# Kernel optimization log

Measured on AMD Instinct MI355X. Metric: run time of the kernel, lower is better.

The kernel has to match this reference:

```python
import jax, jax.numpy as jnp
import numpy as np

B, C, T, N = 8, 128, 12, 4096
E_HALF = 131072
EPS = 1e-5


def _linear_params(key, fan_in, fan_out):
    kw, kb = jax.random.split(key)
    bound = 1.0 / np.sqrt(fan_in)
    W = jax.random.uniform(kw, (fan_in, fan_out), jnp.float32, -bound, bound)
    b = jax.random.uniform(kb, (fan_out,), jnp.float32, -bound, bound)
    return W, b


def setup_inputs() -> dict:
    key = jax.random.key(0)
    ks = jax.random.split(key, 10)
    h_in = jax.random.normal(ks[0], (B, C, T, N), jnp.float32)
    # symmetric edge list: random pairs + reverses + self loops
    u = jax.random.randint(ks[1], (E_HALF,), 0, N, jnp.int32)
    v = jax.random.randint(ks[2], (E_HALF,), 0, N, jnp.int32)
    loops = jnp.arange(N, dtype=jnp.int32)
    row = jnp.concatenate([u, v, loops])
    col = jnp.concatenate([v, u, loops])
    edge_index = jnp.stack([row, col])  # [2, E]
    Wq, bq = _linear_params(ks[3], C, C)
    Wk, bk = _linear_params(ks[4], C, C)
    Wv, bv = _linear_params(ks[5], C, C)
    W1, b1 = _linear_params(ks[6], 2 * C, 4 * C)
    W2, b2 = _linear_params(ks[7], 4 * C, C)
    W3, b3 = _linear_params(ks[8], C, 1)
    return dict(h_in=h_in, edge_index=edge_index, Wq=Wq, bq=bq, Wk=Wk, bk=bk,
                Wv=Wv, bv=bv, W1=W1, b1=b1, W2=W2, b2=b2, W3=W3, b3=b3)


def _masked_instance_norm(x, mask_f):
    # stats over the non-self-loop edges only (matching torch, where the MLP
    # only sees edge_index[:, non_self_loop_mask])
    cnt = mask_f.sum()
    mean = (x * mask_f).sum(0) / cnt
    var = (((x - mean) ** 2) * mask_f).sum(0) / cnt
    return (x - mean) / jnp.sqrt(var + EPS)


def _forward(h_in, edge_index, Wq, bq, Wk, bk, Wv, bv, W1, b1, W2, b2, W3, b3):
    # ---- TemporalAttention ----
    x = jnp.transpose(h_in, (0, 3, 2, 1))  # [B, N, T, C]
    q = x @ Wq + bq
    k = x @ Wk + bk
    v = x @ Wv + bv
    scores = jnp.einsum('bntc,bnsc->bnts', q, k) / (C ** 0.5)
    attn = jax.nn.softmax(scores, axis=-1)
    weighted = jnp.einsum('bnts,bnsc->bntc', attn, v)
    emb = weighted.sum(axis=2)          # [B, N, C]
    emb_mean = emb.mean(axis=0)         # [N, C]

    # ---- ExtractorMLP on non-self-loop edges ----
    row, col = edge_index[0], edge_index[1]
    self_loop = row == col
    mask_f = (~self_loop).astype(emb_mean.dtype)[:, None]  # [E, 1]
    f12 = jnp.concatenate([emb_mean[row], emb_mean[col]], axis=-1)  # [E, 2C]
    h = jax.nn.relu(_masked_instance_norm(f12 @ W1 + b1, mask_f))
    h = jax.nn.relu(_masked_instance_norm(h @ W2 + b2, mask_f))
    logits = h @ W3 + b3                 # [E, 1]

    # concrete_sample, eval mode (deterministic)
    att = jax.nn.sigmoid(logits)
    all_att = jnp.where(self_loop[:, None], 1.0, att)  # [E, 1]

    # ---- transpose + reorder_like: match each edge with its reverse ----
    M = jnp.max(edge_index) + 1
    fwd_key = row * M + col
    rev_key = col * M + row
    order = jnp.argsort(fwd_key)
    pos = jnp.searchsorted(fwd_key[order], rev_key)
    perm = order[pos]                    # index of reverse edge
    edge_att = (all_att + all_att[perm]) * 0.5
    return edge_att


def reference(h_in, edge_index, Wq, bq, Wk, bk, Wv, bv, W1, b1, W2, b2, W3, b3):
    return _forward(h_in, edge_index, Wq, bq, Wk, bk, Wv, bv, W1, b1, W2, b2, W3, b3)
```

## Files before the change

### kernel.cpp

```cpp
#include <hip/hip_runtime.h>
#include <hip/hip_bf16.h>

#define CC     128
#define TT     12
#define NNODE  4096
#define NE     266240
#define EHALF  131072
#define F1     512
#define EPS    1e-5f
#define RSQRTC 0.08838834764831845f
#define EBG    48
#define NBLKG2 5547
#define NF2B   87
#define ST     40

#define O_XWM   0ull
#define O_ICNT  524288ull
#define O_CNT   524416ull
#define O_T     528512ull
#define O_S     528640ull
#define O_T2    545024ull
#define O_GTB   561408ull
#define O_W0B   569600ull
#define O_WC1   569664ull
#define O_WC2   635200ull
#define O_B1C   700736ull
#define O_M1    701248ull
#define O_IS1   701760ull
#define O_M2    702272ull
#define O_IS2   702400ull
#define O_W2T   702528ull
#define O_PB    735296ull
#define O_QB    1783872ull
#define O_ALLA  2832448ull
#define O_PART  3098688ull
#define O_PART2 4518720ull
#define O_Z2    4540992ull

typedef __attribute__((ext_vector_type(8))) short bf16x8;
typedef __attribute__((ext_vector_type(4))) float f32x4;

__device__ inline float bfbits2f(unsigned int v) { return __uint_as_float(v << 16); }
__device__ inline unsigned short f2bf(float x) {
  union { __hip_bfloat16 h; unsigned short u; } cv;
  cv.h = __float2bfloat16(x);
  return cv.u;
}
__device__ inline float f4get(const float4& v, int k) {
  return k == 0 ? v.x : k == 1 ? v.y : k == 2 ? v.z : v.w;
}

__global__ void k_pre(const float* __restrict__ Wq, const float* __restrict__ bq,
                      const float* __restrict__ Wk,
                      unsigned short* __restrict__ Gtb, unsigned short* __restrict__ w0b) {
  int i = blockIdx.x, j = threadIdx.x;
  float acc = 0.f;
  for (int co = 0; co < CC; ++co) acc = fmaf(Wq[i*CC+co], Wk[j*CC+co], acc);
  Gtb[j*CC + i] = f2bf(acc);
  if (j == 0) {
    float a = 0.f;
    for (int co = 0; co < CC; ++co) a = fmaf(Wk[i*CC+co], bq[co], a);
    w0b[i] = f2bf(a);
  }
}

__global__ __launch_bounds__(256) void k_prew(const float* __restrict__ Wv,
    const float* __restrict__ bv, const float* __restrict__ W1, const float* __restrict__ b1,
    float* __restrict__ Wc1, float* __restrict__ Wc2, float* __restrict__ b1c) {
  __shared__ float wvr[CC];
  const int c = blockIdx.x, tid = threadIdx.x;
  if (tid < CC) wvr[tid] = Wv[(size_t)c*CC + tid];
  __syncthreads();
  for (int h = 0; h < 2; ++h) {
    int f = h*256 + tid;
    float a1 = 0.f, a2 = 0.f;
    for (int j = 0; j < CC; ++j) {
      float wv = wvr[j];
      a1 = fmaf(wv, W1[(size_t)j*F1 + f], a1);
      a2 = fmaf(wv, W1[(size_t)(CC + j)*F1 + f], a2);
    }
    Wc1[(size_t)c*F1 + f] = a1;
    Wc2[(size_t)c*F1 + f] = a2;
  }
  if (c == 0) {
    for (int h = 0; h < 2; ++h) {
      int f = h*256 + tid;
      float s = b1[f];
      for (int j = 0; j < CC; ++j)
        s = fmaf(12.f*bv[j], W1[(size_t)j*F1 + f] + W1[(size_t)(CC + j)*F1 + f], s);
      b1c[f] = s;
    }
  }
}

__global__ void k_w2t(const float* __restrict__ W2, unsigned short* __restrict__ W2T) {
  int n = blockIdx.x;
  for (int k = threadIdx.x; k < F1; k += 256)
    W2T[(size_t)n*F1 + k] = f2bf(W2[(size_t)k*CC + n]);
}

__global__ __launch_bounds__(256) void k_hist(const int* __restrict__ row,
    const int* __restrict__ col, int* __restrict__ cnt, int* __restrict__ icnt) {
  __shared__ int h[NNODE];
  const int tid = threadIdx.x;
  for (int i = tid; i < NNODE; i += 256) h[i] = 0;
  __syncthreads();
  int lc = 0;
  const int base = blockIdx.x << 12;
  for (int i = tid; i < 4096; i += 256) {
    int e = base + i;
    int r = row[e], c = col[e];
    if (r != c) { atomicAdd(&h[r], 1); ++lc; }
  }
  #pragma unroll
  for (int d = 1; d < 64; d <<= 1) lc += __shfl_xor(lc, d);
  __syncthreads();
  for (int i = tid; i < NNODE; i += 256) { int v = h[i]; if (v) atomicAdd(&cnt[i], v); }
  if ((tid & 63) == 0) atomicAdd(icnt, lc);
}

__global__ __launch_bounds__(256, 8) void k_attn(
    const float* __restrict__ h_in,
    const unsigned short* __restrict__ Gtb,
    const unsigned short* __restrict__ w0b,
    float* __restrict__ xwm) {
  __shared__ unsigned short xs[48*128];
  __shared__ unsigned short ys[48*128];
  const int tid = threadIdx.x;
  const int bid = ((blockIdx.x & 7) << 10) | (blockIdx.x >> 3);
  const int b  = bid >> 10;
  const int n0 = (bid & 1023) << 2;

  const int w = tid >> 6, lane = tid & 63;
  const int l15 = lane & 15, l4 = lane >> 4;

  {
    const int c2 = tid & 63;
    const float* g0 = h_in + (((size_t)b*CC + 2*c2)*TT + w)*NNODE + n0;
    float4 av[3], bv[3];
    #pragma unroll
    for (int it = 0; it < 3; ++it) {
      av[it] = *(const float4*)(g0 + (size_t)(4*it)*NNODE);
      bv[it] = *(const float4*)(g0 + (size_t)(TT + 4*it)*NNODE);
    }
    #pragma unroll
    for (int it = 0; it < 3; ++it) {
      int t = w + it*4;
      #pragma unroll
      for (int i = 0; i < 4; ++i) {
        float xa = f4get(av[it], i);
        float xb = f4get(bv[it], i);
        int r = i*TT + t;
        unsigned byte = ((unsigned)r << 8) + (((unsigned)(c2*4)) ^ (((unsigned)(r & 7)) << 4));
        *(unsigned*)((char*)xs + byte) = (unsigned)f2bf(xa) | ((unsigned)f2bf(xb) << 16);
      }
    }
  }
  __syncthreads();

  {
    f32x4 acc[2][3];
    #pragma unroll
    for (int mt = 0; mt < 2; ++mt)
      #pragma unroll
      for (int nt = 0; nt < 3; ++nt) acc[mt][nt] = (f32x4){0.f,0.f,0.f,0.f};

    #pragma unroll
    for (int kt = 0; kt < 4; ++kt) {
      bf16x8 gf[2];
      #pragma unroll
      for (int mt = 0; mt < 2; ++mt)
        gf[mt] = *(const bf16x8*)(Gtb + (size_t)((w<<5) + (mt<<4) + l15)*CC + (kt<<5) + (l4<<3));
      bf16x8 bfr[3];
      #pragma unroll
      for (int nt = 0; nt < 3; ++nt) {
        int rr = nt*16 + l15;
        unsigned byte = ((unsigned)rr << 8) +
                        (((unsigned)((kt<<6) + (l4<<4))) ^ (((unsigned)(rr & 7)) << 4));
        bfr[nt] = *(const bf16x8*)((const char*)xs + byte);
      }
      #pragma unroll
      for (int mt = 0; mt < 2; ++mt)
        #pragma unroll
        for (int nt = 0; nt < 3; ++nt)
          acc[mt][nt] = __builtin_amdgcn_mfma_f32_16x16x32_bf16(gf[mt], bfr[nt], acc[mt][nt], 0, 0, 0);
    }
    #pragma unroll
    for (int mt = 0; mt < 2; ++mt)
      #pragma unroll
      for (int nt = 0; nt < 3; ++nt) {
        int rr = nt*16 + l15;
        ushort4 v;
        v.x = f2bf(acc[mt][nt][0]); v.y = f2bf(acc[mt][nt][1]);
        v.z = f2bf(acc[mt][nt][2]); v.w = f2bf(acc[mt][nt][3]);
        unsigned cb = (unsigned)((w<<6) + (mt<<5) + (l4<<3));
        unsigned byte = ((unsigned)rr << 8) + (cb ^ (((unsigned)(rr & 7)) << 4));
        *(ushort4*)((char*)ys + byte) = v;
      }
  }
  __syncthreads();

  {
    const int rb = w*TT;
    const bool sval = (l15 < TT);
    const int rr = rb + (sval ? l15 : 0);
    f32x4 sa = (f32x4){0.f,0.f,0.f,0.f};
    #pragma unroll
    for (int kt = 0; kt < 4; ++kt) {
      unsigned byte = ((unsigned)rr << 8) +
                      (((unsigned)((kt<<6) + (l4<<4))) ^ (((unsigned)(rr & 7)) << 4));
      bf16x8 afr = *(const bf16x8*)((const char*)ys + byte);
      bf16x8 bfr = *(const bf16x8*)((const char*)xs + byte);
      sa = __builtin_amdgcn_mfma_f32_16x16x32_bf16(afr, bfr, sa, 0, 0, 0);
    }
    float dloc = 0.f;
    #pragma unroll
    for (int u = 0; u < 4; ++u) {
      unsigned cb = (unsigned)((l4 << 6) + (u << 4));
      unsigned byte = ((unsigned)rr << 8) + (cb ^ (((unsigned)(rr & 7)) << 4));
      bf16x8 xv = *(const bf16x8*)((const char*)xs + byte);
      bf16x8 wv = *(const bf16x8*)(w0b + (l4 << 5) + (u << 3));
      #pragma unroll
      for (int k = 0; k < 8; ++k)
        dloc = fmaf(bfbits2f((unsigned short)xv[k]), bfbits2f((unsigned short)wv[k]), dloc);
    }
    dloc += __shfl_xor(dloc, 16);
    dloc += __shfl_xor(dloc, 32);
    const float dv = dloc;
    float p[4];
    #pragma unroll
    for (int r = 0; r < 4; ++r) {
      float t1 = sval ? (sa[r] + dv) * RSQRTC : -1e30f;
      float m = t1;
      m = fmaxf(m, __shfl_xor(m, 1));
      m = fmaxf(m, __shfl_xor(m, 2));
      m = fmaxf(m, __shfl_xor(m, 4));
      m = fmaxf(m, __shfl_xor(m, 8));
      float e = exp2f((t1 - m) * 1.4426950408889634f);
      float s = e;
      s += __shfl_xor(s, 1);
      s += __shfl_xor(s, 2);
      s += __shfl_xor(s, 4);
      s += __shfl_xor(s, 8);
      p[r] = e / s;
    }
    float wpart = (l4 < 3) ? (p[0] + p[1] + p[2] + p[3]) : 0.f;
    wpart += __shfl_xor(wpart, 16);
    wpart += __shfl_xor(wpart, 32);
    float xw0 = 0.f, xw1 = 0.f;
    #pragma unroll
    for (int s = 0; s < TT; ++s) {
      float wv = __shfl(wpart, s);
      int r2 = rb + s;
      unsigned byte = ((unsigned)r2 << 8) +
                      (((unsigned)(lane << 2)) ^ (((unsigned)(r2 & 7)) << 4));
      unsigned xp = *(const unsigned*)((const char*)xs + byte);
      xw0 = fmaf(wv, bfbits2f(xp & 0xffffu), xw0);
      xw1 = fmaf(wv, bfbits2f(xp >> 16), xw1);
    }
    unsafeAtomicAdd(&xwm[(size_t)(n0 + w)*CC + (lane << 1)],     xw0 * 0.125f);
    unsafeAtomicAdd(&xwm[(size_t)(n0 + w)*CC + (lane << 1) + 1], xw1 * 0.125f);
  }
}

__global__ __launch_bounds__(256) void k_S(const float* __restrict__ xwm,
    const int* __restrict__ row, const int* __restrict__ col, float* __restrict__ S) {
  __shared__ unsigned short XT[128*ST];
  __shared__ unsigned short YT[128*ST];
  const int tid = threadIdx.x;
  const int w = tid >> 6, lane = tid & 63, l15 = lane & 15, l4 = lane >> 4;
  const int j = tid & 31, fi = tid >> 5;
  const int f0 = fi << 4;
  f32x4 acc[2][8];
  #pragma unroll
  for (int mt = 0; mt < 2; ++mt)
    #pragma unroll
    for (int nt = 0; nt < 8; ++nt) acc[mt][nt] = (f32x4){0.f,0.f,0.f,0.f};

  const int ebase = blockIdx.x << 9;
  for (int bt = 0; bt < 16; ++bt) {
    const int e = ebase + (bt << 5) + j;
    const int r = row[e], c = col[e];
    const bool msk = (r != c);
    const float* xr = xwm + (size_t)r*CC + f0;
    const float* xc = xwm + (size_t)c*CC + f0;
    float4 xv[4], yv[4];
    #pragma unroll
    for (int u = 0; u < 4; ++u) { xv[u] = *(const float4*)(xr + 4*u); yv[u] = *(const float4*)(xc + 4*u); }
    __syncthreads();
    #pragma unroll
    for (int u = 0; u < 16; ++u) {
      float xvv = f4get(xv[u >> 2], u & 3);
      float yvv = f4get(yv[u >> 2], u & 3);
      XT[(f0+u)*ST + j] = f2bf(xvv);
      YT[(f0+u)*ST + j] = msk ? f2bf(yvv) : (unsigned short)0;
    }
    __syncthreads();
    bf16x8 af[2];
    #pragma unroll
    for (int mt = 0; mt < 2; ++mt)
      af[mt] = *(const bf16x8*)&XT[((((w<<1)+mt)<<4) + l15)*ST + (l4<<3)];
    #pragma unroll
    for (int nt = 0; nt < 8; ++nt) {
      bf16x8 bf_ = *(const bf16x8*)&YT[(((nt<<4) + l15))*ST + (l4<<3)];
      acc[0][nt] = __builtin_amdgcn_mfma_f32_16x16x32_bf16(af[0], bf_, acc[0][nt], 0, 0, 0);
      acc[1][nt] = __builtin_amdgcn_mfma_f32_16x16x32_bf16(af[1], bf_, acc[1][nt], 0, 0, 0);
    }
  }
  #pragma unroll
  for (int mt = 0; mt < 2; ++mt)
    #pragma unroll
    for (int nt = 0; nt < 8; ++nt)
      #pragma unroll
      for (int reg = 0; reg < 4; ++reg) {
        int a = (((w<<1)+mt)<<4) + (l4<<2) + reg;
        int b = (nt<<4) + l15;
        unsafeAtomicAdd(&S[a*128 + b], acc[mt][nt][reg]);
      }
}

__global__ __launch_bounds__(256) void k_T2(const float* __restrict__ xwm,
    const int* __restrict__ cnt, float* __restrict__ T2, float* __restrict__ t) {
  __shared__ unsigned short XT[128*ST];
  __shared__ unsigned short YT[128*ST];
  __shared__ float tl[128];
  const int tid = threadIdx.x;
  const int w = tid >> 6, lane = tid & 63, l15 = lane & 15, l4 = lane >> 4;
  const int j = tid & 31, fi = tid >> 5;
  const int f0 = fi << 4;
  if (tid < 128) tl[tid] = 0.f;
  f32x4 acc[2][8];
  #pragma unroll
  for (int mt = 0; mt < 2; ++mt)
    #pragma unroll
    for (int nt = 0; nt < 8; ++nt) acc[mt][nt] = (f32x4){0.f,0.f,0.f,0.f};
  float tloc[16];
  #pragma unroll
  for (int u = 0; u < 16; ++u) tloc[u] = 0.f;

  const int nbase = blockIdx.x << 7;
  for (int bt = 0; bt < 4; ++bt) {
    const int n = nbase + (bt << 5) + j;
    const float cw = (float)cnt[n];
    const float* xr = xwm + (size_t)n*CC + f0;
    float4 xv[4];
    #pragma unroll
    for (int u = 0; u < 4; ++u) xv[u] = *(const float4*)(xr + 4*u);
    __syncthreads();
    #pragma unroll
    for (int u = 0; u < 16; ++u) {
      float xvv = f4get(xv[u >> 2], u & 3);
      float yvv = cw * xvv;
      XT[(f0+u)*ST + j] = f2bf(xvv);
      YT[(f0+u)*ST + j] = f2bf(yvv);
      tloc[u] += yvv;
    }
    __syncthreads();
    bf16x8 af[2];
    #pragma unroll
    for (int mt = 0; mt < 2; ++mt)
      af[mt] = *(const bf16x8*)&XT[((((w<<1)+mt)<<4) + l15)*ST + (l4<<3)];
    #pragma unroll
    for (int nt = 0; nt < 8; ++nt) {
      bf16x8 bf_ = *(const bf16x8*)&YT[(((nt<<4) + l15))*ST + (l4<<3)];
      acc[0][nt] = __builtin_amdgcn_mfma_f32_16x16x32_bf16(af[0], bf_, acc[0][nt], 0, 0, 0);
      acc[1][nt] = __builtin_amdgcn_mfma_f32_16x16x32_bf16(af[1], bf_, acc[1][nt], 0, 0, 0);
    }
  }
  #pragma unroll
  for (int u = 0; u < 16; ++u) atomicAdd(&tl[f0 + u], tloc[u]);
  #pragma unroll
  for (int mt = 0; mt < 2; ++mt)
    #pragma unroll
    for (int nt = 0; nt < 8; ++nt)
      #pragma unroll
      for (int reg = 0; reg < 4; ++reg) {
        int a = (((w<<1)+mt)<<4) + (l4<<2) + reg;
        int b = (nt<<4) + l15;
        unsafeAtomicAdd(&T2[a*128 + b], acc[mt][nt][reg]);
      }
  __syncthreads();
  if (tid < 128) unsafeAtomicAdd(&t[tid], tl[tid]);
}

__global__ __launch_bounds__(128) void k_stats(const float* __restrict__ S,
    const float* __restrict__ T2, const float* __restrict__ Wc1,
    const float* __restrict__ Wc2, const float* __restrict__ b1c,
    const float* __restrict__ t, const int* __restrict__ icnt,
    float* __restrict__ m1, float* __restrict__ is1) {
  __shared__ float w1c[128], w2c[128];
  __shared__ float redq[2], redt1[2], redt2[2];
  const int f = blockIdx.x, a = threadIdx.x;
  w1c[a] = Wc1[(size_t)a*F1 + f];
  w2c[a] = Wc2[(size_t)a*F1 + f];
  __syncthreads();
  float v1 = 0.f, v2 = 0.f, v3 = 0.f;
  const float* Sr = S + a*128;
  const float* Tr = T2 + a*128;
  for (int b = 0; b < 128; b += 4) {
    float4 sv = *(const float4*)(Sr + b);
    float4 tv = *(const float4*)(Tr + b);
    float4 w1v = *(const float4*)&w1c[b];
    float4 w2v = *(const float4*)&w2c[b];
    #pragma unroll
    for (int u = 0; u < 4; ++u) {
      v1 = fmaf(f4get(sv, u), f4get(w2v, u), v1);
      v2 = fmaf(f4get(tv, u), f4get(w1v, u), v2);
      v3 = fmaf(f4get(tv, u), f4get(w2v, u), v3);
    }
  }
  float pa  = w1c[a]*(v2 + 2.f*v1) + w2c[a]*v3;
  float ta1 = t[a]*w1c[a];
  float ta2 = t[a]*w2c[a];
  #pragma unroll
  for (int d = 1; d < 64; d <<= 1) {
    pa  += __shfl_xor(pa, d);
    ta1 += __shfl_xor(ta1, d);
    ta2 += __shfl_xor(ta2, d);
  }
  if ((a & 63) == 0) { redq[a>>6] = pa; redt1[a>>6] = ta1; redt2[a>>6] = ta2; }
  __syncthreads();
  if (a == 0) {
    float cntf = (float)(*icnt);
    float bb = b1c[f];
    float sumq = redq[0] + redq[1];
    float st1 = redt1[0] + redt1[1];
    float st2 = redt2[0] + redt2[1];
    float w2tot = sumq + 2.f*bb*(st1 + st2) + cntf*bb*bb;
    float w1tot = st1 + st2 + cntf*bb;
    float m = w1tot / cntf;
    m1[f] = m;
    is1[f] = rsqrtf(w2tot/cntf - m*m + EPS);
  }
}

__global__ __launch_bounds__(256) void k_pq(const float* __restrict__ xwm,
    const float* __restrict__ Wc1, const float* __restrict__ Wc2,
    const float* __restrict__ b1c, const float* __restrict__ m1,
    const float* __restrict__ is1,
    unsigned short* __restrict__ Pb, unsigned short* __restrict__ Qb) {
  __shared__ float em[4][CC];
  const int tid = threadIdx.x;
  const int n0 = blockIdx.x << 2;
  for (int i = tid; i < 4*CC; i += 256)
    em[i >> 7][i & 127] = xwm[(size_t)(n0 + (i >> 7))*CC + (i & 127)];
  __syncthreads();
  for (int half = 0; half < 2; ++half) {
    const int f = half*256 + tid;
    const float mm = m1[f], ii = is1[f], bb = b1c[f];
    for (int nn = 0; nn < 4; ++nn) {
      float ap = bb, aq = 0.f;
      for (int c = 0; c < CC; ++c) {
        float e = em[nn][c];
        ap = fmaf(e, Wc1[(size_t)c*F1 + f], ap);
        aq = fmaf(e, Wc2[(size_t)c*F1 + f], aq);
      }
      Pb[(size_t)(n0+nn)*F1 + f] = f2bf(ap * ii);
      Qb[(size_t)(n0+nn)*F1 + f] = f2bf((aq - mm) * ii);
    }
  }
}

__global__ __launch_bounds__(512, 6) void k_gemm(const unsigned short* __restrict__ Pb,
    const unsigned short* __restrict__ Qb, const int* __restrict__ row,
    const int* __restrict__ col,
    const unsigned short* __restrict__ W2T, const float* __restrict__ b2,
    unsigned short* __restrict__ z2, float* __restrict__ part) {
  __shared__ unsigned short h1s[EBG*F1];
  __shared__ int rS[EBG], cS[EBG]; __shared__ float mk[EBG];
  __shared__ float cstat[256];
  const int tid = threadIdx.x;
  const int bid = blockIdx.x;
  const int e0 = bid * EBG;
  const int w = tid >> 6, lane = tid & 63;
  const int wn0 = w << 4;
  const int l15 = lane & 15, l4 = lane >> 4;
  if (tid < EBG) {
    int e = e0 + tid;
    bool valid = e < NE;
    int r = valid ? row[e] : 0, c = valid ? col[e] : 0;
    rS[tid] = r; cS[tid] = c; mk[tid] = (valid && r != c) ? 1.f : 0.f;
  }
  __syncthreads();

  #pragma unroll
  for (int rr = 0; rr < 2; ++rr) {
    int jj[3], cc[3];
    #pragma unroll
    for (int s = 0; s < 3; ++s) {
      int i = tid + ((rr*3 + s) << 9);
      jj[s] = i >> 6; cc[s] = i & 63;
    }
    uint4 pv[3], qv[3];
    #pragma unroll
    for (int s = 0; s < 3; ++s) pv[s] = *(const uint4*)(Pb + (size_t)rS[jj[s]]*F1 + (cc[s] << 3));
    #pragma unroll
    for (int s = 0; s < 3; ++s) qv[s] = *(const uint4*)(Qb + (size_t)cS[jj[s]]*F1 + (cc[s] << 3));
    #pragma unroll
    for (int s = 0; s < 3; ++s) {
      unsigned out[4];
      #pragma unroll
      for (int q = 0; q < 4; ++q) {
        unsigned pu = (&pv[s].x)[q], qu = (&qv[s].x)[q];
        float ha = fmaxf(bfbits2f(pu & 0xffffu) + bfbits2f(qu & 0xffffu), 0.f);
        float hb = fmaxf(bfbits2f(pu >> 16)     + bfbits2f(qu >> 16),     0.f);
        out[q] = (unsigned)f2bf(ha) | ((unsigned)f2bf(hb) << 16);
      }
      unsigned byte = ((unsigned)jj[s] << 10) +
                      (((unsigned)(cc[s] << 4)) ^ (((unsigned)(jj[s] & 7)) << 4));
      *(uint4*)((char*)h1s + byte) = make_uint4(out[0], out[1], out[2], out[3]);
    }
  }
  __syncthreads();

  f32x4 acc[3];
  #pragma unroll
  for (int a = 0; a < 3; ++a) acc[a] = (f32x4){0.f,0.f,0.f,0.f};

  const unsigned short* w2p = W2T + (size_t)(wn0 + l15)*F1 + (l4 << 3);
  #pragma unroll
  for (int kt = 0; kt < 16; ++kt) {
    bf16x8 bfr = *(const bf16x8*)(w2p + (kt << 5));
    bf16x8 afr[3];
    #pragma unroll
    for (int mt = 0; mt < 3; ++mt) {
      int j = (mt << 4) + l15;
      unsigned byte = ((unsigned)j << 10) + (((unsigned)(kt*64 + l4*16)) ^ ((j & 7) << 4));
      afr[mt] = *(const bf16x8*)((const char*)h1s + byte);
    }
    #pragma unroll
    for (int mt = 0; mt < 3; ++mt)
      acc[mt] = __builtin_amdgcn_mfma_f32_16x16x32_bf16(afr[mt], bfr, acc[mt], 0, 0, 0);
  }
  __syncthreads();

  float* z2s = (float*)&h1s[0];
  const int colg = wn0 + l15;
  {
    float bb = b2[colg];
    float sloc = 0.f, qloc = 0.f;
    #pragma unroll
    for (int mt = 0; mt < 3; ++mt) {
      f32x4 v = acc[mt];
      #pragma unroll
      for (int reg = 0; reg < 4; ++reg) {
        int j = (mt << 4) + (l4 << 2) + reg;
        float z = v[reg] + bb;
        float m = mk[j];
        sloc = fmaf(m, z, sloc);
        qloc = fmaf(m*z, z, qloc);
        z2s[j*132 + colg] = z;
      }
    }
    sloc += __shfl_xor(sloc, 16); sloc += __shfl_xor(sloc, 32);
    qloc += __shfl_xor(qloc, 16); qloc += __shfl_xor(qloc, 32);
    if (l4 == 0) { cstat[colg] = sloc; cstat[128 + colg] = qloc; }
  }
  __syncthreads();

  #pragma unroll
  for (int p = 0; p < 2; ++p) {
    int idx = (p << 12) + (tid << 3);
    if (idx < EBG*CC) {
      int j = idx >> 7, c = idx & 127;
      if (e0 + j < NE) {
        const float* src = &z2s[j*132 + c];
        float4 v0 = *(const float4*)src;
        float4 v1 = *(const float4*)(src + 4);
        uint4 o;
        o.x = (unsigned)f2bf(v0.x) | ((unsigned)f2bf(v0.y) << 16);
        o.y = (unsigned)f2bf(v0.z) | ((unsigned)f2bf(v0.w) << 16);
        o.z = (unsigned)f2bf(v1.x) | ((unsigned)f2bf(v1.y) << 16);
        o.w = (unsigned)f2bf(v1.z) | ((unsigned)f2bf(v1.w) << 16);
        *(uint4*)(z2 + (size_t)e0*CC + idx) = o;
      }
    }
  }
  if (tid < 256) part[(size_t)bid*256 + tid] = cstat[tid];
}

__global__ __launch_bounds__(256) void k_fin2a(const float* __restrict__ part,
                                               float* __restrict__ part2) {
  const int g = blockIdx.x, tid = threadIdx.x;
  float s = 0.f;
  for (int r = 0; r < 64; ++r) {
    int b = g*64 + r;
    if (b < NBLKG2) s += part[(size_t)b*256 + tid];
  }
  part2[(size_t)g*256 + tid] = s;
}

__global__ __launch_bounds__(256) void k_fin2b(const float* __restrict__ part2,
    const int* __restrict__ icnt, float* __restrict__ m2, float* __restrict__ is2) {
  __shared__ float red[256];
  const int tid = threadIdx.x;
  float s = 0.f;
  for (int g = 0; g < NF2B; ++g) s += part2[(size_t)g*256 + tid];
  red[tid] = s;
  __syncthreads();
  if (tid < 128) {
    float cnt = (float)(*icnt);
    float m = red[tid] / cnt;
    m2[tid] = m;
    is2[tid] = rsqrtf(red[128 + tid]/cnt - m*m + EPS);
  }
}

__global__ __launch_bounds__(256) void k_score(const unsigned short* __restrict__ z2,
    const int* __restrict__ row, const int* __restrict__ col,
    const float* __restrict__ m2, const float* __restrict__ is2,
    const float* __restrict__ W3, const float* __restrict__ b3,
    float* __restrict__ all_att) {
  __shared__ float zt[64][129];
  const int tid = threadIdx.x;
  const int e0 = blockIdx.x << 6;
  const uint4* src = reinterpret_cast<const uint4*>(z2 + (size_t)e0*CC);
  for (int i = tid; i < 64*CC/8; i += 256) {
    uint4 v = src[i];
    int flat = i*8;
    int j = flat >> 7, k = flat & 127;
    zt[j][k+0] = bfbits2f(v.x & 0xffffu); zt[j][k+1] = bfbits2f(v.x >> 16);
    zt[j][k+2] = bfbits2f(v.y & 0xffffu); zt[j][k+3] = bfbits2f(v.y >> 16);
    zt[j][k+4] = bfbits2f(v.z & 0xffffu); zt[j][k+5] = bfbits2f(v.z >> 16);
    zt[j][k+6] = bfbits2f(v.w & 0xffffu); zt[j][k+7] = bfbits2f(v.w >> 16);
  }
  __syncthreads();
  const int j = tid >> 2, q = tid & 3;
  float a = 0.f;
  for (int k = q*32; k < q*32 + 32; ++k)
    a = fmaf(fmaxf((zt[j][k] - m2[k])*is2[k], 0.f), W3[k], a);
  a += __shfl_xor(a, 1, 4);
  a += __shfl_xor(a, 2, 4);
  if (q == 0) {
    int e = e0 + j;
    int r = row[e], c = col[e];
    float att;
    if (r == c) att = 1.f;
    else        att = 1.f / (1.f + expf(-(a + b3[0])));
    all_att[e] = att;
  }
}

__global__ __launch_bounds__(256) void k_out(const float* __restrict__ all_att,
    float* __restrict__ out) {
  int e = blockIdx.x*256 + threadIdx.x;
  int p = (e < EHALF) ? (e + EHALF) : (e < 2*EHALF ? e - EHALF : e);
  out[e] = 0.5f * (all_att[e] + all_att[p]);
}

extern "C" void kernel_launch(void* const* d_in, const int* in_sizes, int n_in,
                              void* d_out, int out_size, void* d_ws, size_t ws_size,
                              hipStream_t stream) {
  const float* h_in = (const float*)d_in[0];
  const int*   ei   = (const int*)d_in[1];
  const float* Wq = (const float*)d_in[2];
  const float* bq = (const float*)d_in[3];
  const float* Wk = (const float*)d_in[4];
  const float* bk = (const float*)d_in[5];  (void)bk;
  const float* Wv = (const float*)d_in[6];
  const float* bv = (const float*)d_in[7];
  const float* W1 = (const float*)d_in[8];
  const float* b1 = (const float*)d_in[9];
  const float* W2 = (const float*)d_in[10];
  const float* b2 = (const float*)d_in[11];
  const float* W3 = (const float*)d_in[12];
  const float* b3 = (const float*)d_in[13];
  float* ws = (float*)d_ws;
  float* out = (float*)d_out;
  const int* row = ei;
  const int* col = ei + NE;

  hipMemsetAsync(ws, 0, 561408ull * 4ull, stream);

  k_pre<<<128, 128, 0, stream>>>(Wq, bq, Wk,
                                 (unsigned short*)(ws+O_GTB), (unsigned short*)(ws+O_W0B));
  k_prew<<<128, 256, 0, stream>>>(Wv, bv, W1, b1, ws+O_WC1, ws+O_WC2, ws+O_B1C);
  k_w2t<<<128, 256, 0, stream>>>(W2, (unsigned short*)(ws+O_W2T));
  k_hist<<<64, 256, 0, stream>>>(row, col, (int*)(ws+O_CNT), (int*)(ws+O_ICNT));
  k_attn<<<8192, 256, 0, stream>>>(h_in, (const unsigned short*)(ws+O_GTB),
                                   (const unsigned short*)(ws+O_W0B), ws+O_XWM);
  k_S<<<512, 256, 0, stream>>>(ws+O_XWM, row, col, ws+O_S);
  k_T2<<<32, 256, 0, stream>>>(ws+O_XWM, (const int*)(ws+O_CNT), ws+O_T2, ws+O_T);
  k_stats<<<512, 128, 0, stream>>>(ws+O_S, ws+O_T2, ws+O_WC1, ws+O_WC2, ws+O_B1C,
                                   ws+O_T, (const int*)(ws+O_ICNT), ws+O_M1, ws+O_IS1);
  k_pq<<<1024, 256, 0, stream>>>(ws+O_XWM, ws+O_WC1, ws+O_WC2, ws+O_B1C,
                                 ws+O_M1, ws+O_IS1,
                                 (unsigned short*)(ws+O_PB), (unsigned short*)(ws+O_QB));
  k_gemm<<<NBLKG2, 512, 0, stream>>>((const unsigned short*)(ws+O_PB),
                                     (const unsigned short*)(ws+O_QB), row, col,
                                     (const unsigned short*)(ws+O_W2T), b2,
                                     (unsigned short*)(ws+O_Z2), ws+O_PART);
  k_fin2a<<<NF2B, 256, 0, stream>>>(ws+O_PART, ws+O_PART2);
  k_fin2b<<<1, 256, 0, stream>>>(ws+O_PART2, (const int*)(ws+O_ICNT), ws+O_M2, ws+O_IS2);
  k_score<<<4160, 256, 0, stream>>>((const unsigned short*)(ws+O_Z2), row, col,
                                    ws+O_M2, ws+O_IS2, W3, b3, ws+O_ALLA);
  k_out<<<1040, 256, 0, stream>>>(ws+O_ALLA, out);
}
```

Measured before the change: 503.5 us.

## Merge setup kernels, fold bias dot into MFMA, atomic stats, streamline scoring

Merges the four setup kernels into one launch and k_S/k_T2 into one launch. The k_attn bias dot product becomes an extra MFMA row, and the softmax max subtraction is dropped. The two-stage partial-sum reduction after the GEMM is replaced by global atomics. k_score is rewritten to read z2 directly without LDS staging, using a precomputed scale times W3. This cuts launch count, reduction passes and instruction work, but skipping the max subtraction risks exp overflow and float atomics make sums order-dependent.

```diff
diff --git a/kernel.cpp b/kernel.cpp
--- a/kernel.cpp
+++ b/kernel.cpp
@@ -9,9 +9,9 @@
 #define F1     512
 #define EPS    1e-5f
 #define RSQRTC 0.08838834764831845f
+#define LOG2E  1.4426950408889634f
 #define EBG    48
 #define NBLKG2 5547
-#define NF2B   87
 #define ST     40
 
 #define O_XWM   0ull
@@ -20,22 +20,21 @@
 #define O_T     528512ull
 #define O_S     528640ull
 #define O_T2    545024ull
-#define O_GTB   561408ull
-#define O_W0B   569600ull
-#define O_WC1   569664ull
-#define O_WC2   635200ull
-#define O_B1C   700736ull
-#define O_M1    701248ull
-#define O_IS1   701760ull
-#define O_M2    702272ull
-#define O_IS2   702400ull
-#define O_W2T   702528ull
-#define O_PB    735296ull
-#define O_QB    1783872ull
-#define O_ALLA  2832448ull
-#define O_PART  3098688ull
-#define O_PART2 4518720ull
-#define O_Z2    4540992ull
+#define O_STAT2 561408ull
+#define O_GTB   561664ull
+#define O_W0B   569856ull
+#define O_WC1   569920ull
+#define O_WC2   635456ull
+#define O_B1C   700992ull
+#define O_M1    701504ull
+#define O_IS1   702016ull
+#define O_M2    702528ull
+#define O_AW    702656ull
+#define O_W2T   702784ull
+#define O_PB    735552ull
+#define O_QB    1784128ull
+#define O_ALLA  2832704ull
+#define O_Z2    3098944ull
 
 typedef __attribute__((ext_vector_type(8))) short bf16x8;
 typedef __attribute__((ext_vector_type(4))) float f32x4;
@@ -50,73 +49,74 @@
   return k == 0 ? v.x : k == 1 ? v.y : k == 2 ? v.z : v.w;
 }
 
-__global__ void k_pre(const float* __restrict__ Wq, const float* __restrict__ bq,
-                      const float* __restrict__ Wk,
-                      unsigned short* __restrict__ Gtb, unsigned short* __restrict__ w0b) {
-  int i = blockIdx.x, j = threadIdx.x;
-  float acc = 0.f;
-  for (int co = 0; co < CC; ++co) acc = fmaf(Wq[i*CC+co], Wk[j*CC+co], acc);
-  Gtb[j*CC + i] = f2bf(acc);
-  if (j == 0) {
-    float a = 0.f;
-    for (int co = 0; co < CC; ++co) a = fmaf(Wk[i*CC+co], bq[co], a);
-    w0b[i] = f2bf(a);
-  }
-}
-
-__global__ __launch_bounds__(256) void k_prew(const float* __restrict__ Wv,
-    const float* __restrict__ bv, const float* __restrict__ W1, const float* __restrict__ b1,
-    float* __restrict__ Wc1, float* __restrict__ Wc2, float* __restrict__ b1c) {
+__global__ __launch_bounds__(256) void k_setup(
+    const float* __restrict__ Wq, const float* __restrict__ bq,
+    const float* __restrict__ Wk, const float* __restrict__ Wv,
+    const float* __restrict__ bv, const float* __restrict__ W1,
+    const float* __restrict__ b1, const float* __restrict__ W2,
+    const int* __restrict__ row, const int* __restrict__ col,
+    unsigned short* __restrict__ Gtb, unsigned short* __restrict__ w0b,
+    float* __restrict__ Wc1, float* __restrict__ Wc2, float* __restrict__ b1c,
+    unsigned short* __restrict__ W2T, int* __restrict__ cnt, int* __restrict__ icnt) {
   __shared__ float wvr[CC];
-  const int c = blockIdx.x, tid = threadIdx.x;
-  if (tid < CC) wvr[tid] = Wv[(size_t)c*CC + tid];
-  __syncthreads();
-  for (int h = 0; h < 2; ++h) {
-    int f = h*256 + tid;
-    float a1 = 0.f, a2 = 0.f;
-    for (int j = 0; j < CC; ++j) {
-      float wv = wvr[j];
-      a1 = fmaf(wv, W1[(size_t)j*F1 + f], a1);
-      a2 = fmaf(wv, W1[(size_t)(CC + j)*F1 + f], a2);
-    }
-    Wc1[(size_t)c*F1 + f] = a1;
-    Wc2[(size_t)c*F1 + f] = a2;
-  }
-  if (c == 0) {
-    for (int h = 0; h < 2; ++h) {
-      int f = h*256 + tid;
-      float s = b1[f];
-      for (int j = 0; j < CC; ++j)
-        s = fmaf(12.f*bv[j], W1[(size_t)j*F1 + f] + W1[(size_t)(CC + j)*F1 + f], s);
-      b1c[f] = s;
-    }
-  }
-}
-
-__global__ void k_w2t(const float* __restrict__ W2, unsigned short* __restrict__ W2T) {
-  int n = blockIdx.x;
-  for (int k = threadIdx.x; k < F1; k += 256)
-    W2T[(size_t)n*F1 + k] = f2bf(W2[(size_t)k*CC + n]);
-}
-
-__global__ __launch_bounds__(256) void k_hist(const int* __restrict__ row,
-    const int* __restrict__ col, int* __restrict__ cnt, int* __restrict__ icnt) {
   __shared__ int h[NNODE];
-  const int tid = threadIdx.x;
-  for (int i = tid; i < NNODE; i += 256) h[i] = 0;
-  __syncthreads();
-  int lc = 0;
-  const int base = blockIdx.x << 12;
-  for (int i = tid; i < 4096; i += 256) {
-    int e = base + i;
-    int r = row[e], c = col[e];
-    if (r != c) { atomicAdd(&h[r], 1); ++lc; }
-  }
-  #pragma unroll
-  for (int d = 1; d < 64; d <<= 1) lc += __shfl_xor(lc, d);
-  __syncthreads();
-  for (int i = tid; i < NNODE; i += 256) { int v = h[i]; if (v) atomicAdd(&cnt[i], v); }
-  if ((tid & 63) == 0) atomicAdd(icnt, lc);
+  const int blk = blockIdx.x, tid = threadIdx.x;
+  if (blk < 128) {
+    if (tid < 128) {
+      int i = blk, j = tid;
+      float acc = 0.f;
+      for (int co = 0; co < CC; ++co) acc = fmaf(Wq[i*CC+co], Wk[j*CC+co], acc);
+      Gtb[j*CC + i] = f2bf(acc);
+      if (j == 0) {
+        float a = 0.f;
+        for (int co = 0; co < CC; ++co) a = fmaf(Wk[i*CC+co], bq[co], a);
+        w0b[i] = f2bf(a);
+      }
+    }
+  } else if (blk < 256) {
+    const int c = blk - 128;
+    if (tid < CC) wvr[tid] = Wv[(size_t)c*CC + tid];
+    __syncthreads();
+    for (int hh = 0; hh < 2; ++hh) {
+      int f = hh*256 + tid;
+      float a1 = 0.f, a2 = 0.f;
+      for (int j = 0; j < CC; ++j) {
+        float wv = wvr[j];
+        a1 = fmaf(wv, W1[(size_t)j*F1 + f], a1);
+        a2 = fmaf(wv, W1[(size_t)(CC + j)*F1 + f], a2);
+      }
+      Wc1[(size_t)c*F1 + f] = a1;
+      Wc2[(size_t)c*F1 + f] = a2;
+    }
+    if (c == 0) {
+      for (int hh = 0; hh < 2; ++hh) {
+        int f = hh*256 + tid;
+        float s = b1[f];
+        for (int j = 0; j < CC; ++j)
+          s = fmaf(12.f*bv[j], W1[(size_t)j*F1 + f] + W1[(size_t)(CC + j)*F1 + f], s);
+        b1c[f] = s;
+      }
+    }
+  } else if (blk < 384) {
+    const int n = blk - 256;
+    for (int k = tid; k < F1; k += 256)
+      W2T[(size_t)n*F1 + k] = f2bf(W2[(size_t)k*CC + n]);
+  } else {
+    for (int i = tid; i < NNODE; i += 256) h[i] = 0;
+    __syncthreads();
+    int lc = 0;
+    const int base = (blk - 384) << 12;
+    for (int i = tid; i < 4096; i += 256) {
+      int e = base + i;
+      int r = row[e], c = col[e];
+      if (r != c) { atomicAdd(&h[r], 1); ++lc; }
+    }
+    #pragma unroll
+    for (int d = 1; d < 64; d <<= 1) lc += __shfl_xor(lc, d);
+    __syncthreads();
+    for (int i = tid; i < NNODE; i += 256) { int v = h[i]; if (v) atomicAdd(&cnt[i], v); }
+    if ((tid & 63) == 0) atomicAdd(icnt, lc);
+  }
 }
 
 __global__ __launch_bounds__(256, 8) void k_attn(
@@ -125,7 +125,7 @@
     const unsigned short* __restrict__ w0b,
     float* __restrict__ xwm) {
   __shared__ unsigned short xs[48*128];
-  __shared__ unsigned short ys[48*128];
+  __shared__ unsigned short ys[49*128];
   const int tid = threadIdx.x;
   const int bid = ((blockIdx.x & 7) << 10) | (blockIdx.x >> 3);
   const int b  = bid >> 10;
@@ -142,6 +142,10 @@
     for (int it = 0; it < 3; ++it) {
       av[it] = *(const float4*)(g0 + (size_t)(4*it)*NNODE);
       bv[it] = *(const float4*)(g0 + (size_t)(TT + 4*it)*NNODE);
+    }
+    if (tid < 16) {
+      uint4 wv = *(const uint4*)(w0b + (tid << 3));
+      *(uint4*)((char*)ys + 48*256 + (tid << 4)) = wv;
     }
     #pragma unroll
     for (int it = 0; it < 3; ++it) {
@@ -203,40 +207,24 @@
   {
     const int rb = w*TT;
     const bool sval = (l15 < TT);
-    const int rr = rb + (sval ? l15 : 0);
+    const int rr  = rb + (sval ? l15 : 0);
+    const int rra = sval ? (rb + l15) : 48;
     f32x4 sa = (f32x4){0.f,0.f,0.f,0.f};
     #pragma unroll
     for (int kt = 0; kt < 4; ++kt) {
-      unsigned byte = ((unsigned)rr << 8) +
-                      (((unsigned)((kt<<6) + (l4<<4))) ^ (((unsigned)(rr & 7)) << 4));
-      bf16x8 afr = *(const bf16x8*)((const char*)ys + byte);
-      bf16x8 bfr = *(const bf16x8*)((const char*)xs + byte);
+      unsigned kb = (unsigned)((kt<<6) + (l4<<4));
+      unsigned byteA = ((unsigned)rra << 8) + (kb ^ (((unsigned)(rra & 7)) << 4));
+      unsigned byteB = ((unsigned)rr  << 8) + (kb ^ (((unsigned)(rr  & 7)) << 4));
+      bf16x8 afr = *(const bf16x8*)((const char*)ys + byteA);
+      bf16x8 bfr = *(const bf16x8*)((const char*)xs + byteB);
       sa = __builtin_amdgcn_mfma_f32_16x16x32_bf16(afr, bfr, sa, 0, 0, 0);
     }
-    float dloc = 0.f;
-    #pragma unroll
-    for (int u = 0; u < 4; ++u) {
-      unsigned cb = (unsigned)((l4 << 6) + (u << 4));
-      unsigned byte = ((unsigned)rr << 8) + (cb ^ (((unsigned)(rr & 7)) << 4));
-      bf16x8 xv = *(const bf16x8*)((const char*)xs + byte);
-      bf16x8 wv = *(const bf16x8*)(w0b + (l4 << 5) + (u << 3));
-      #pragma unroll
-      for (int k = 0; k < 8; ++k)
-        dloc = fmaf(bfbits2f((unsigned short)xv[k]), bfbits2f((unsigned short)wv[k]), dloc);
-    }
-    dloc += __shfl_xor(dloc, 16);
-    dloc += __shfl_xor(dloc, 32);
-    const float dv = dloc;
+    float dv = __shfl(sa[0], 48 + l15);
     float p[4];
     #pragma unroll
     for (int r = 0; r < 4; ++r) {
       float t1 = sval ? (sa[r] + dv) * RSQRTC : -1e30f;
-      float m = t1;
-      m = fmaxf(m, __shfl_xor(m, 1));
-      m = fmaxf(m, __shfl_xor(m, 2));
-      m = fmaxf(m, __shfl_xor(m, 4));
-      m = fmaxf(m, __shfl_xor(m, 8));
-      float e = exp2f((t1 - m) * 1.4426950408889634f);
+      float e = exp2f(t1 * LOG2E);
       float s = e;
       s += __shfl_xor(s, 1);
       s += __shfl_xor(s, 2);
@@ -263,10 +251,13 @@
   }
 }
 
-__global__ __launch_bounds__(256) void k_S(const float* __restrict__ xwm,
-    const int* __restrict__ row, const int* __restrict__ col, float* __restrict__ S) {
+__global__ __launch_bounds__(256) void k_ST2(const float* __restrict__ xwm,
+    const int* __restrict__ row, const int* __restrict__ col,
+    const int* __restrict__ cnt, float* __restrict__ S,
+    float* __restrict__ T2, float* __restrict__ t) {
   __shared__ unsigned short XT[128*ST];
   __shared__ unsigned short YT[128*ST];
+  __shared__ float tl[128];
   const int tid = threadIdx.x;
   const int w = tid >> 6, lane = tid & 63, l15 = lane & 15, l4 = lane >> 4;
   const int j = tid & 31, fi = tid >> 5;
@@ -277,110 +268,96 @@
     #pragma unroll
     for (int nt = 0; nt < 8; ++nt) acc[mt][nt] = (f32x4){0.f,0.f,0.f,0.f};
 
-  const int ebase = blockIdx.x << 9;
-  for (int bt = 0; bt < 16; ++bt) {
-    const int e = ebase + (bt << 5) + j;
-    const int r = row[e], c = col[e];
-    const bool msk = (r != c);
-    const float* xr = xwm + (size_t)r*CC + f0;
-    const float* xc = xwm + (size_t)c*CC + f0;
-    float4 xv[4], yv[4];
-    #pragma unroll
-    for (int u = 0; u < 4; ++u) { xv[u] = *(const float4*)(xr + 4*u); yv[u] = *(const float4*)(xc + 4*u); }
+  if (blockIdx.x < 512) {
+    const int ebase = blockIdx.x << 9;
+    for (int bt = 0; bt < 16; ++bt) {
+      const int e = ebase + (bt << 5) + j;
+      const int r = row[e], c = col[e];
+      const bool msk = (r != c);
+      const float* xr = xwm + (size_t)r*CC + f0;
+      const float* xc = xwm + (size_t)c*CC + f0;
+      float4 xv[4], yv[4];
+      #pragma unroll
+      for (int u = 0; u < 4; ++u) { xv[u] = *(const float4*)(xr + 4*u); yv[u] = *(const float4*)(xc + 4*u); }
+      __syncthreads();
+      #pragma unroll
+      for (int u = 0; u < 16; ++u) {
+        float xvv = f4get(xv[u >> 2], u & 3);
+        float yvv = f4get(yv[u >> 2], u & 3);
+        XT[(f0+u)*ST + j] = f2bf(xvv);
+        YT[(f0+u)*ST + j] = msk ? f2bf(yvv) : (unsigned short)0;
+      }
+      __syncthreads();
+      bf16x8 af[2];
+      #pragma unroll
+      for (int mt = 0; mt < 2; ++mt)
+        af[mt] = *(const bf16x8*)&XT[((((w<<1)+mt)<<4) + l15)*ST + (l4<<3)];
+      #pragma unroll
+      for (int nt = 0; nt < 8; ++nt) {
+        bf16x8 bf_ = *(const bf16x8*)&YT[(((nt<<4) + l15))*ST + (l4<<3)];
+        acc[0][nt] = __builtin_amdgcn_mfma_f32_16x16x32_bf16(af[0], bf_, acc[0][nt], 0, 0, 0);
+        acc[1][nt] = __builtin_amdgcn_mfma_f32_16x16x32_bf16(af[1], bf_, acc[1][nt], 0, 0, 0);
+      }
+    }
+    #pragma unroll
+    for (int mt = 0; mt < 2; ++mt)
+      #pragma unroll
+      for (int nt = 0; nt < 8; ++nt)
+        #pragma unroll
+        for (int reg = 0; reg < 4; ++reg) {
+          int a = (((w<<1)+mt)<<4) + (l4<<2) + reg;
+          int b = (nt<<4) + l15;
+          unsafeAtomicAdd(&S[a*128 + b], acc[mt][nt][reg]);
+        }
+  } else {
+    if (tid < 128) tl[tid] = 0.f;
+    float tloc[16];
+    #pragma unroll
+    for (int u = 0; u < 16; ++u) tloc[u] = 0.f;
+    const int nbase = (blockIdx.x - 512) << 7;
+    for (int bt = 0; bt < 4; ++bt) {
+      const int n = nbase + (bt << 5) + j;
+      const float cw = (float)cnt[n];
+      const float* xr = xwm + (size_t)n*CC + f0;
+      float4 xv[4];
+      #pragma unroll
+      for (int u = 0; u < 4; ++u) xv[u] = *(const float4*)(xr + 4*u);
+      __syncthreads();
+      #pragma unroll
+      for (int u = 0; u < 16; ++u) {
+        float xvv = f4get(xv[u >> 2], u & 3);
+        float yvv = cw * xvv;
+        XT[(f0+u)*ST + j] = f2bf(xvv);
+        YT[(f0+u)*ST + j] = f2bf(yvv);
+        tloc[u] += yvv;
+      }
+      __syncthreads();
+      bf16x8 af[2];
+      #pragma unroll
+      for (int mt = 0; mt < 2; ++mt)
+        af[mt] = *(const bf16x8*)&XT[((((w<<1)+mt)<<4) + l15)*ST + (l4<<3)];
+      #pragma unroll
+      for (int nt = 0; nt < 8; ++nt) {
+        bf16x8 bf_ = *(const bf16x8*)&YT[(((nt<<4) + l15))*ST + (l4<<3)];
+        acc[0][nt] = __builtin_amdgcn_mfma_f32_16x16x32_bf16(af[0], bf_, acc[0][nt], 0, 0, 0);
+        acc[1][nt] = __builtin_amdgcn_mfma_f32_16x16x32_bf16(af[1], bf_, acc[1][nt], 0, 0, 0);
+      }
+    }
+    #pragma unroll
+    for (int u = 0; u < 16; ++u) atomicAdd(&tl[f0 + u], tloc[u]);
+    #pragma unroll
+    for (int mt = 0; mt < 2; ++mt)
+      #pragma unroll
+      for (int nt = 0; nt < 8; ++nt)
+        #pragma unroll
+        for (int reg = 0; reg < 4; ++reg) {
+          int a = (((w<<1)+mt)<<4) + (l4<<2) + reg;
+          int b = (nt<<4) + l15;
+          unsafeAtomicAdd(&T2[a*128 + b], acc[mt][nt][reg]);
+        }
     __syncthreads();
-    #pragma unroll
-    for (int u = 0; u < 16; ++u) {
-      float xvv = f4get(xv[u >> 2], u & 3);
-      float yvv = f4get(yv[u >> 2], u & 3);
-      XT[(f0+u)*ST + j] = f2bf(xvv);
-      YT[(f0+u)*ST + j] = msk ? f2bf(yvv) : (unsigned short)0;
-    }
-    __syncthreads();
-    bf16x8 af[2];
-    #pragma unroll
-    for (int mt = 0; mt < 2; ++mt)
-      af[mt] = *(const bf16x8*)&XT[((((w<<1)+mt)<<4) + l15)*ST + (l4<<3)];
-    #pragma unroll
-    for (int nt = 0; nt < 8; ++nt) {
-      bf16x8 bf_ = *(const bf16x8*)&YT[(((nt<<4) + l15))*ST + (l4<<3)];
-      acc[0][nt] = __builtin_amdgcn_mfma_f32_16x16x32_bf16(af[0], bf_, acc[0][nt], 0, 0, 0);
-      acc[1][nt] = __builtin_amdgcn_mfma_f32_16x16x32_bf16(af[1], bf_, acc[1][nt], 0, 0, 0);
-    }
-  }
-  #pragma unroll
-  for (int mt = 0; mt < 2; ++mt)
-    #pragma unroll
-    for (int nt = 0; nt < 8; ++nt)
-      #pragma unroll
-      for (int reg = 0; reg < 4; ++reg) {
-        int a = (((w<<1)+mt)<<4) + (l4<<2) + reg;
-        int b = (nt<<4) + l15;
-        unsafeAtomicAdd(&S[a*128 + b], acc[mt][nt][reg]);
-      }
-}
-
-__global__ __launch_bounds__(256) void k_T2(const float* __restrict__ xwm,
-    const int* __restrict__ cnt, float* __restrict__ T2, float* __restrict__ t) {
-  __shared__ unsigned short XT[128*ST];
-  __shared__ unsigned short YT[128*ST];
-  __shared__ float tl[128];
-  const int tid = threadIdx.x;
-  const int w = tid >> 6, lane = tid & 63, l15 = lane & 15, l4 = lane >> 4;
-  const int j = tid & 31, fi = tid >> 5;
-  const int f0 = fi << 4;
-  if (tid < 128) tl[tid] = 0.f;
-  f32x4 acc[2][8];
-  #pragma unroll
-  for (int mt = 0; mt < 2; ++mt)
-    #pragma unroll
-    for (int nt = 0; nt < 8; ++nt) acc[mt][nt] = (f32x4){0.f,0.f,0.f,0.f};
-  float tloc[16];
-  #pragma unroll
-  for (int u = 0; u < 16; ++u) tloc[u] = 0.f;
-
-  const int nbase = blockIdx.x << 7;
-  for (int bt = 0; bt < 4; ++bt) {
-    const int n = nbase + (bt << 5) + j;
-    const float cw = (float)cnt[n];
-    const float* xr = xwm + (size_t)n*CC + f0;
-    float4 xv[4];
-    #pragma unroll
-    for (int u = 0; u < 4; ++u) xv[u] = *(const float4*)(xr + 4*u);
-    __syncthreads();
-    #pragma unroll
-    for (int u = 0; u < 16; ++u) {
-      float xvv = f4get(xv[u >> 2], u & 3);
-      float yvv = cw * xvv;
-      XT[(f0+u)*ST + j] = f2bf(xvv);
-      YT[(f0+u)*ST + j] = f2bf(yvv);
-      tloc[u] += yvv;
-    }
-    __syncthreads();
-    bf16x8 af[2];
-    #pragma unroll
-    for (int mt = 0; mt < 2; ++mt)
-      af[mt] = *(const bf16x8*)&XT[((((w<<1)+mt)<<4) + l15)*ST + (l4<<3)];
-    #pragma unroll
-    for (int nt = 0; nt < 8; ++nt) {
-      bf16x8 bf_ = *(const bf16x8*)&YT[(((nt<<4) + l15))*ST + (l4<<3)];
-      acc[0][nt] = __builtin_amdgcn_mfma_f32_16x16x32_bf16(af[0], bf_, acc[0][nt], 0, 0, 0);
-      acc[1][nt] = __builtin_amdgcn_mfma_f32_16x16x32_bf16(af[1], bf_, acc[1][nt], 0, 0, 0);
-    }
-  }
-  #pragma unroll
-  for (int u = 0; u < 16; ++u) atomicAdd(&tl[f0 + u], tloc[u]);
-  #pragma unroll
-  for (int mt = 0; mt < 2; ++mt)
-    #pragma unroll
-    for (int nt = 0; nt < 8; ++nt)
-      #pragma unroll
-      for (int reg = 0; reg < 4; ++reg) {
-        int a = (((w<<1)+mt)<<4) + (l4<<2) + reg;
-        int b = (nt<<4) + l15;
-        unsafeAtomicAdd(&T2[a*128 + b], acc[mt][nt][reg]);
-      }
-  __syncthreads();
-  if (tid < 128) unsafeAtomicAdd(&t[tid], tl[tid]);
+    if (tid < 128) unsafeAtomicAdd(&t[tid], tl[tid]);
+  }
 }
 
 __global__ __launch_bounds__(128) void k_stats(const float* __restrict__ S,
@@ -465,7 +442,7 @@
     const unsigned short* __restrict__ Qb, const int* __restrict__ row,
     const int* __restrict__ col,
     const unsigned short* __restrict__ W2T, const float* __restrict__ b2,
-    unsigned short* __restrict__ z2, float* __restrict__ part) {
+    unsigned short* __restrict__ z2, float* __restrict__ stat2) {
   __shared__ unsigned short h1s[EBG*F1];
   __shared__ int rS[EBG], cS[EBG]; __shared__ float mk[EBG];
   __shared__ float cstat[256];
@@ -576,68 +553,60 @@
       }
     }
   }
-  if (tid < 256) part[(size_t)bid*256 + tid] = cstat[tid];
-}
-
-__global__ __launch_bounds__(256) void k_fin2a(const float* __restrict__ part,
-                                               float* __restrict__ part2) {
-  const int g = blockIdx.x, tid = threadIdx.x;
-  float s = 0.f;
-  for (int r = 0; r < 64; ++r) {
-    int b = g*64 + r;
-    if (b < NBLKG2) s += part[(size_t)b*256 + tid];
-  }
-  part2[(size_t)g*256 + tid] = s;
-}
-
-__global__ __launch_bounds__(256) void k_fin2b(const float* __restrict__ part2,
-    const int* __restrict__ icnt, float* __restrict__ m2, float* __restrict__ is2) {
-  __shared__ float red[256];
-  const int tid = threadIdx.x;
-  float s = 0.f;
-  for (int g = 0; g < NF2B; ++g) s += part2[(size_t)g*256 + tid];
-  red[tid] = s;
-  __syncthreads();
-  if (tid < 128) {
-    float cnt = (float)(*icnt);
-    float m = red[tid] / cnt;
-    m2[tid] = m;
-    is2[tid] = rsqrtf(red[128 + tid]/cnt - m*m + EPS);
-  }
+  if (tid < 256) unsafeAtomicAdd(&stat2[tid], cstat[tid]);
+}
+
+__global__ void k_fin2(const float* __restrict__ stat2, const int* __restrict__ icnt,
+                       const float* __restrict__ W3,
+                       float* __restrict__ m2, float* __restrict__ aw) {
+  int f = threadIdx.x;
+  float cnt = (float)(*icnt);
+  float m = stat2[f] / cnt;
+  m2[f] = m;
+  aw[f] = rsqrtf(stat2[128 + f]/cnt - m*m + EPS) * W3[f];
 }
 
 __global__ __launch_bounds__(256) void k_score(const unsigned short* __restrict__ z2,
     const int* __restrict__ row, const int* __restrict__ col,
-    const float* __restrict__ m2, const float* __restrict__ is2,
-    const float* __restrict__ W3, const float* __restrict__ b3,
-    float* __restrict__ all_att) {
-  __shared__ float zt[64][129];
+    const float* __restrict__ m2, const float* __restrict__ aw,
+    const float* __restrict__ b3, float* __restrict__ all_att) {
   const int tid = threadIdx.x;
-  const int e0 = blockIdx.x << 6;
-  const uint4* src = reinterpret_cast<const uint4*>(z2 + (size_t)e0*CC);
-  for (int i = tid; i < 64*CC/8; i += 256) {
-    uint4 v = src[i];
-    int flat = i*8;
-    int j = flat >> 7, k = flat & 127;
-    zt[j][k+0] = bfbits2f(v.x & 0xffffu); zt[j][k+1] = bfbits2f(v.x >> 16);
-    zt[j][k+2] = bfbits2f(v.y & 0xffffu); zt[j][k+3] = bfbits2f(v.y >> 16);
-    zt[j][k+4] = bfbits2f(v.z & 0xffffu); zt[j][k+5] = bfbits2f(v.z >> 16);
-    zt[j][k+6] = bfbits2f(v.w & 0xffffu); zt[j][k+7] = bfbits2f(v.w >> 16);
-  }
-  __syncthreads();
-  const int j = tid >> 2, q = tid & 3;
-  float a = 0.f;
-  for (int k = q*32; k < q*32 + 32; ++k)
-    a = fmaf(fmaxf((zt[j][k] - m2[k])*is2[k], 0.f), W3[k], a);
-  a += __shfl_xor(a, 1, 4);
-  a += __shfl_xor(a, 2, 4);
-  if (q == 0) {
-    int e = e0 + j;
-    int r = row[e], c = col[e];
-    float att;
-    if (r == c) att = 1.f;
-    else        att = 1.f / (1.f + expf(-(a + b3[0])));
-    all_att[e] = att;
+  const int w = tid >> 6, lane = tid & 63;
+  const int g = lane >> 4, sub = lane & 15;
+  const int f0 = sub << 3;
+  float mv[8], av[8];
+  {
+    float4 a0 = *(const float4*)(m2 + f0);
+    float4 a1 = *(const float4*)(m2 + f0 + 4);
+    float4 b0 = *(const float4*)(aw + f0);
+    float4 b1 = *(const float4*)(aw + f0 + 4);
+    #pragma unroll
+    for (int u = 0; u < 4; ++u) { mv[u] = f4get(a0, u); mv[4+u] = f4get(a1, u); }
+    #pragma unroll
+    for (int u = 0; u < 4; ++u) { av[u] = f4get(b0, u); av[4+u] = f4get(b1, u); }
+  }
+  const float bb = b3[0];
+  #pragma unroll
+  for (int it = 0; it < 4; ++it) {
+    const int e = (blockIdx.x << 6) + (w << 4) + (it << 2) + g;
+    uint4 zv = *(const uint4*)(z2 + (size_t)e*CC + f0);
+    float a = 0.f;
+    #pragma unroll
+    for (int u = 0; u < 4; ++u) {
+      unsigned zu = (&zv.x)[u];
+      float z0 = bfbits2f(zu & 0xffffu);
+      float z1 = bfbits2f(zu >> 16);
+      a += (z0 > mv[2*u])   ? (z0 - mv[2*u])*av[2*u]     : 0.f;
+      a += (z1 > mv[2*u+1]) ? (z1 - mv[2*u+1])*av[2*u+1] : 0.f;
+    }
+    a += __shfl_xor(a, 1);
+    a += __shfl_xor(a, 2);
+    a += __shfl_xor(a, 4);
+    a += __shfl_xor(a, 8);
+    if (sub == 0) {
+      int r = row[e], c = col[e];
+      all_att[e] = (r == c) ? 1.f : 1.f/(1.f + expf(-(a + bb)));
+    }
   }
 }
 
@@ -670,17 +639,17 @@
   const int* row = ei;
   const int* col = ei + NE;
 
-  hipMemsetAsync(ws, 0, 561408ull * 4ull, stream);
-
-  k_pre<<<128, 128, 0, stream>>>(Wq, bq, Wk,
-                                 (unsigned short*)(ws+O_GTB), (unsigned short*)(ws+O_W0B));
-  k_prew<<<128, 256, 0, stream>>>(Wv, bv, W1, b1, ws+O_WC1, ws+O_WC2, ws+O_B1C);
-  k_w2t<<<128, 256, 0, stream>>>(W2, (unsigned short*)(ws+O_W2T));
-  k_hist<<<64, 256, 0, stream>>>(row, col, (int*)(ws+O_CNT), (int*)(ws+O_ICNT));
+  hipMemsetAsync(ws, 0, 561664ull * 4ull, stream);
+
+  k_setup<<<448, 256, 0, stream>>>(Wq, bq, Wk, Wv, bv, W1, b1, W2, row, col,
+                                   (unsigned short*)(ws+O_GTB), (unsigned short*)(ws+O_W0B),
+                                   ws+O_WC1, ws+O_WC2, ws+O_B1C,
+                                   (unsigned short*)(ws+O_W2T),
+                                   (int*)(ws+O_CNT), (int*)(ws+O_ICNT));
   k_attn<<<8192, 256, 0, stream>>>(h_in, (const unsigned short*)(ws+O_GTB),
                                    (const unsigned short*)(ws+O_W0B), ws+O_XWM);
-  k_S<<<512, 256, 0, stream>>>(ws+O_XWM, row, col, ws+O_S);
-  k_T2<<<32, 256, 0, stream>>>(ws+O_XWM, (const int*)(ws+O_CNT), ws+O_T2, ws+O_T);
+  k_ST2<<<544, 256, 0, stream>>>(ws+O_XWM, row, col, (const int*)(ws+O_CNT),
+                                 ws+O_S, ws+O_T2, ws+O_T);
   k_stats<<<512, 128, 0, stream>>>(ws+O_S, ws+O_T2, ws+O_WC1, ws+O_WC2, ws+O_B1C,
                                    ws+O_T, (const int*)(ws+O_ICNT), ws+O_M1, ws+O_IS1);
   k_pq<<<1024, 256, 0, stream>>>(ws+O_XWM, ws+O_WC1, ws+O_WC2, ws+O_B1C,
@@ -689,10 +658,10 @@
   k_gemm<<<NBLKG2, 512, 0, stream>>>((const unsigned short*)(ws+O_PB),
                                      (const unsigned short*)(ws+O_QB), row, col,
                                      (const unsigned short*)(ws+O_W2T), b2,
-                                     (unsigned short*)(ws+O_Z2), ws+O_PART);
-  k_fin2a<<<NF2B, 256, 0, stream>>>(ws+O_PART, ws+O_PART2);
-  k_fin2b<<<1, 256, 0, stream>>>(ws+O_PART2, (const int*)(ws+O_ICNT), ws+O_M2, ws+O_IS2);
+                                     (unsigned short*)(ws+O_Z2), ws+O_STAT2);
+  k_fin2<<<1, 128, 0, stream>>>(ws+O_STAT2, (const int*)(ws+O_ICNT), W3,
+                                ws+O_M2, ws+O_AW);
   k_score<<<4160, 256, 0, stream>>>((const unsigned short*)(ws+O_Z2), row, col,
-                                    ws+O_M2, ws+O_IS2, W3, b3, ws+O_ALLA);
+                                    ws+O_M2, ws+O_AW, b3, ws+O_ALLA);
   k_out<<<1040, 256, 0, stream>>>(ws+O_ALLA, out);
 }
```

New measurement: 461.8 us. 8.3% less time.
